# Kernel tuning notes

Hardware: AMD Instinct MI355X
Metric: run time of the kernel (lower is better)

Reference implementation:

```python
import jax, jax.numpy as jnp
import numpy as np

B, S, D, E = 4, 2048, 512, 32

def setup_inputs() -> dict:
    key = jax.random.key(0)
    k1, k2, k3 = jax.random.split(key, 3)
    x = jax.random.normal(k1, (B, S, D), dtype=jnp.float32)
    # glorot-ish scaling for weights
    gate_w = jax.random.normal(k2, (D, E), dtype=jnp.float32) * (1.0 / np.sqrt(D))
    gate_b = jnp.zeros((E,), dtype=jnp.float32)
    expert_w = jax.random.normal(k3, (E, D, D), dtype=jnp.float32) * (1.0 / np.sqrt(D))
    return {"x": x, "gate_w": gate_w, "gate_b": gate_b, "expert_w": expert_w}

def reference(x, gate_w, gate_b, expert_w):
    # gate_scores: [B,S,E] (context=None -> route on x itself)
    gate = jax.nn.softmax(jnp.einsum('bsd,de->bse', x, gate_w) + gate_b, axis=-1)
    # Dense soft-MoE: sum_e gate[b,s,e] * (x[b,s,:] @ expert_w[e])
    # Single einsum avoids materializing the [B,S,E,D] intermediate.
    out = jnp.einsum('bse,bsd,edf->bsf', gate, x, expert_w)
    return out
```

## Files before the change

kernel.cpp:

```cpp
#include <hip/hip_runtime.h>

#define TOK 8192
#define DIM 512
#define NE  32
#define KTOT (NE * DIM)

#define BM 128
#define BN 128
#define BK 64

typedef float f32x4  __attribute__((ext_vector_type(4)));
typedef float f32x16 __attribute__((ext_vector_type(16)));
typedef short s16x8  __attribute__((ext_vector_type(8)));

typedef const void __attribute__((address_space(1)))* gp1_t;
typedef void __attribute__((address_space(3)))* lp3_t;

__device__ __forceinline__ void gl_lds16(const void* g, void* l) {
    __builtin_amdgcn_global_load_lds((gp1_t)g, (lp3_t)l, 16, 0, 0);
}

__device__ __forceinline__ void stage4(const ushort* g, size_t gstride, char* l) {
    gl_lds16(g,               l);
    gl_lds16(g + gstride,     l + 4096);
    gl_lds16(g + 2 * gstride, l + 8192);
    gl_lds16(g + 3 * gstride, l + 12288);
}

__device__ __forceinline__ ushort f2bf(float f) {
    unsigned u = __builtin_bit_cast(unsigned, f);
    unsigned r = (u + 0x7fffu + ((u >> 16) & 1u)) >> 16;
    return (ushort)r;
}

__global__ __launch_bounds__(256) void k_prep(const float* __restrict__ w,
                                              ushort* __restrict__ wt,
                                              const float* __restrict__ x,
                                              const float* __restrict__ gw,
                                              const float* __restrict__ gb,
                                              float* __restrict__ G,
                                              ushort* __restrict__ xb) {
    __shared__ __align__(16) char smem[64 * 65 * 4];
    const int bx = blockIdx.x;
    const int tid = threadIdx.x;
    if (bx < 2048) {
        float (*tile)[65] = (float(*)[65])smem;
        const int e = bx >> 6;
        const int f0 = ((bx >> 3) & 7) * 64;
        const int d0 = (bx & 7) * 64;
        const int tx = tid & 63, ty = tid >> 6;
        const float* we = w + (size_t)e * DIM * DIM;
#pragma unroll
        for (int i = ty; i < 64; i += 4)
            tile[i][tx] = we[(size_t)(d0 + i) * DIM + f0 + tx];
        __syncthreads();
#pragma unroll
        for (int i = ty; i < 64; i += 4)
            wt[(size_t)(f0 + i) * KTOT + e * DIM + d0 + tx] = f2bf(tile[tx][i]);
    } else {
        float* xs = (float*)smem;
        const int t0 = (bx - 2048) * 8;
        const float* xBase = x + (size_t)t0 * DIM;
#pragma unroll
        for (int k = 0; k < 4; ++k) {
            int i4 = (k * 256 + tid) * 4;
            float4 v = *(const float4*)(xBase + i4);
            xs[i4 + 0] = v.x; xs[i4 + 1] = v.y; xs[i4 + 2] = v.z; xs[i4 + 3] = v.w;
            ushort4 o;
            o.x = f2bf(v.x); o.y = f2bf(v.y); o.z = f2bf(v.z); o.w = f2bf(v.w);
            *(ushort4*)(xb + (size_t)t0 * DIM + i4) = o;
        }
        __syncthreads();
        const int tok = tid >> 5;
        const int e = tid & 31;
        float l = gb[e];
        const float* xr = xs + tok * DIM;
#pragma unroll 8
        for (int d = 0; d < DIM; ++d)
            l += xr[d] * gw[d * NE + e];
        float mx = l;
#pragma unroll
        for (int m = 16; m >= 1; m >>= 1) mx = fmaxf(mx, __shfl_xor(mx, m));
        float ex = expf(l - mx);
        float s = ex;
#pragma unroll
        for (int m = 16; m >= 1; m >>= 1) s += __shfl_xor(s, m);
        G[(size_t)(t0 + tok) * NE + e] = ex / s;
    }
}

__global__ __launch_bounds__(256, 2) void k_moe_gemm(const ushort* __restrict__ xb,
                                                     const ushort* __restrict__ wt,
                                                     const float* __restrict__ G,
                                                     float* __restrict__ out0,
                                                     float* __restrict__ out1) {
    __shared__ __align__(16) ushort As[2][BM * BK];
    __shared__ __align__(16) ushort Bs[2][BN * BK];
    __shared__ float Gs[16][BM];

    const int tid = threadIdx.x;
    const int m0 = blockIdx.y * BM;
    const int n0 = blockIdx.x * BN;
    const int e0 = blockIdx.z * 16;
    float* __restrict__ dst = blockIdx.z ? out1 : out0;

    for (int i = tid; i < 16 * BM; i += 256) {
        int e = i >> 7, r = i & 127;
        Gs[e][r] = G[(size_t)(m0 + r) * NE + e0 + e];
    }

    const int lane = tid & 63;
    const int wave = tid >> 6;
    const int wm = (wave & 1) * 64;
    const int wn = (wave >> 1) * 64;
    const int l31 = lane & 31;
    const int hi = lane >> 5;
    const int key = l31 & 7;

    int chunkOff[4], rowOffA[2], rowOffB[2];
#pragma unroll
    for (int s = 0; s < 4; ++s) chunkOff[s] = ((2 * s + hi) ^ key) * 16;
#pragma unroll
    for (int i = 0; i < 2; ++i) {
        rowOffA[i] = (wm + i * 32 + l31) * 128;
        rowOffB[i] = (wn + i * 32 + l31) * 128;
    }

    const int srow = tid >> 3;
    const int scol = ((tid & 7) ^ (srow & 7)) * 8;
    const ushort* aBase = xb + (size_t)(m0 + srow) * DIM + scol;
    const ushort* bBase = wt + (size_t)(n0 + srow) * KTOT + (size_t)e0 * DIM + scol;
    const int ldsOff = tid * 16;

    f32x16 zv16;
#pragma unroll
    for (int j = 0; j < 16; ++j) zv16[j] = 0.f;
    f32x16 acc[2][2];
#pragma unroll
    for (int i = 0; i < 2; ++i)
#pragma unroll
        for (int j = 0; j < 2; ++j) acc[i][j] = zv16;

    stage4(aBase, (size_t)32 * DIM,  (char*)As[0] + ldsOff);
    stage4(bBase, (size_t)32 * KTOT, (char*)Bs[0] + ldsOff);
    __syncthreads();

#pragma unroll 1
    for (int kt = 0; kt < 8; ++kt) {
        const char* Ab = (const char*)As[kt & 1];
        s16x8 areg[2][4];
#pragma unroll
        for (int mi = 0; mi < 2; ++mi)
#pragma unroll
            for (int s = 0; s < 4; ++s)
                areg[mi][s] = *(const s16x8*)(Ab + rowOffA[mi] + chunkOff[s]);

#pragma unroll 1
        for (int ee = 0; ee < 16; ++ee) {
            const int gn = kt * 16 + ee + 1;
            if (gn < 128) {
                const ushort* bN = bBase + (size_t)(gn & 15) * DIM + (gn >> 4) * BK;
                stage4(bN, (size_t)32 * KTOT, (char*)Bs[gn & 1] + ldsOff);
                if (ee == 15)
                    stage4(aBase + (gn >> 4) * BK, (size_t)32 * DIM,
                           (char*)As[(gn >> 4) & 1] + ldsOff);
            }

            const char* Bb = (const char*)Bs[ee & 1];
            s16x8 breg[2][4];
#pragma unroll
            for (int nj = 0; nj < 2; ++nj)
#pragma unroll
                for (int s = 0; s < 4; ++s)
                    breg[nj][s] = *(const s16x8*)(Bb + rowOffB[nj] + chunkOff[s]);

#pragma unroll
            for (int mi = 0; mi < 2; ++mi) {
                f32x16 p0 = __builtin_amdgcn_mfma_f32_32x32x16_bf16(areg[mi][0], breg[0][0], zv16, 0, 0, 0);
                f32x16 p1 = __builtin_amdgcn_mfma_f32_32x32x16_bf16(areg[mi][0], breg[1][0], zv16, 0, 0, 0);
#pragma unroll
                for (int s = 1; s < 4; ++s) {
                    p0 = __builtin_amdgcn_mfma_f32_32x32x16_bf16(areg[mi][s], breg[0][s], p0, 0, 0, 0);
                    p1 = __builtin_amdgcn_mfma_f32_32x32x16_bf16(areg[mi][s], breg[1][s], p1, 0, 0, 0);
                }
#pragma unroll
                for (int g = 0; g < 4; ++g) {
                    const f32x4 gt = *(const f32x4*)&Gs[ee][wm + mi * 32 + 8 * g + 4 * hi];
#pragma unroll
                    for (int j = 0; j < 4; ++j) {
                        acc[mi][0][4 * g + j] += gt[j] * p0[4 * g + j];
                        acc[mi][1][4 * g + j] += gt[j] * p1[4 * g + j];
                    }
                }
            }
            __syncthreads();
        }
    }

#pragma unroll
    for (int mi = 0; mi < 2; ++mi)
#pragma unroll
        for (int nj = 0; nj < 2; ++nj) {
            const int col = n0 + wn + nj * 32 + l31;
#pragma unroll
            for (int g = 0; g < 4; ++g) {
                float* p = dst + (size_t)(m0 + wm + mi * 32 + 8 * g + 4 * hi) * DIM + col;
                p[0 * DIM] = acc[mi][nj][4 * g + 0];
                p[1 * DIM] = acc[mi][nj][4 * g + 1];
                p[2 * DIM] = acc[mi][nj][4 * g + 2];
                p[3 * DIM] = acc[mi][nj][4 * g + 3];
            }
        }
}

__global__ __launch_bounds__(256) void k_reduce(float* __restrict__ out,
                                                const float* __restrict__ P) {
    int i = (blockIdx.x * 256 + threadIdx.x) * 4;
    float4 a = *(const float4*)(out + i);
    float4 b = *(const float4*)(P + i);
    a.x += b.x; a.y += b.y; a.z += b.z; a.w += b.w;
    *(float4*)(out + i) = a;
}

extern "C" void kernel_launch(void* const* d_in, const int* in_sizes, int n_in,
                              void* d_out, int out_size, void* d_ws, size_t ws_size,
                              hipStream_t stream) {
    const float* x  = (const float*)d_in[0];
    const float* gw = (const float*)d_in[1];
    const float* gb = (const float*)d_in[2];
    const float* w  = (const float*)d_in[3];
    float* out = (float*)d_out;

    char* ws = (char*)d_ws;
    ushort* xb = (ushort*)ws;
    ushort* wt = (ushort*)(ws + (8u << 20));
    float*  G  = (float*)(ws + (24u << 20));
    float*  P  = (float*)(ws + (25u << 20));

    k_prep<<<dim3(2048 + TOK / 8), dim3(256), 0, stream>>>(w, wt, x, gw, gb, G, xb);
    k_moe_gemm<<<dim3(DIM / BN, TOK / BM, 2), dim3(256), 0, stream>>>(xb, wt, G, out, P);
    k_reduce<<<dim3(TOK * DIM / 1024), dim3(256), 0, stream>>>(out, P);
}
```

Baseline: 259.9 us.

## Triple-buffer B tiles with prefetch distance two and counted vmcnt waits

The GEMM's B-tile staging moves from double to triple buffering, and loads are issued two iterations ahead. The full __syncthreads is replaced with s_waitcnt vmcnt(N) plus a barrier, so in-flight global-to-LDS loads can keep running across iterations. The A tile becomes single-buffered and is reloaded once per kt, after its registers have been read. This targets memory-latency stalls, at the cost of extra LDS per block, which may reduce occupancy. It also depends on precise vmcnt accounting being correct.

Measured after the change: 284.3 us. +9.4%, slower.

```diff
diff --git a/kernel.cpp b/kernel.cpp
--- a/kernel.cpp
+++ b/kernel.cpp
@@ -25,6 +25,12 @@
     gl_lds16(g + gstride,     l + 4096);
     gl_lds16(g + 2 * gstride, l + 8192);
     gl_lds16(g + 3 * gstride, l + 12288);
+}
+
+template<int N>
+__device__ __forceinline__ void wait_bar() {
+    asm volatile("s_waitcnt vmcnt(%0) lgkmcnt(0)" :: "n"(N) : "memory");
+    __builtin_amdgcn_s_barrier();
 }
 
 __device__ __forceinline__ ushort f2bf(float f) {
@@ -94,8 +100,8 @@
                                                      const float* __restrict__ G,
                                                      float* __restrict__ out0,
                                                      float* __restrict__ out1) {
-    __shared__ __align__(16) ushort As[2][BM * BK];
-    __shared__ __align__(16) ushort Bs[2][BN * BK];
+    __shared__ __align__(16) ushort As[BM * BK];
+    __shared__ __align__(16) ushort Bs[3][BN * BK];
     __shared__ float Gs[16][BM];
 
     const int tid = threadIdx.x;
@@ -141,38 +147,50 @@
 #pragma unroll
         for (int j = 0; j < 2; ++j) acc[i][j] = zv16;
 
-    stage4(aBase, (size_t)32 * DIM,  (char*)As[0] + ldsOff);
+    stage4(aBase, (size_t)32 * DIM, (char*)As + ldsOff);
     stage4(bBase, (size_t)32 * KTOT, (char*)Bs[0] + ldsOff);
-    __syncthreads();
+    stage4(bBase + (size_t)1 * DIM, (size_t)32 * KTOT, (char*)Bs[1] + ldsOff);
+    asm volatile("s_waitcnt vmcnt(0) lgkmcnt(0)" ::: "memory");
+    __builtin_amdgcn_s_barrier();
+
+    char* Br0 = (char*)Bs[0];
+    char* Br1 = (char*)Bs[1];
+    char* Br2 = (char*)Bs[2];
+
+    s16x8 areg[2][4];
 
 #pragma unroll 1
     for (int kt = 0; kt < 8; ++kt) {
-        const char* Ab = (const char*)As[kt & 1];
-        s16x8 areg[2][4];
-#pragma unroll
-        for (int mi = 0; mi < 2; ++mi)
-#pragma unroll
-            for (int s = 0; s < 4; ++s)
-                areg[mi][s] = *(const s16x8*)(Ab + rowOffA[mi] + chunkOff[s]);
-
 #pragma unroll 1
         for (int ee = 0; ee < 16; ++ee) {
-            const int gn = kt * 16 + ee + 1;
+            const int g = kt * 16 + ee;
+
+            if (kt == 7 && ee == 15)                  wait_bar<0>();
+            else if (kt < 7 && (ee == 2 || ee == 3))  wait_bar<8>();
+            else                                      wait_bar<4>();
+
+            const int gn = g + 2;
             if (gn < 128) {
                 const ushort* bN = bBase + (size_t)(gn & 15) * DIM + (gn >> 4) * BK;
-                stage4(bN, (size_t)32 * KTOT, (char*)Bs[gn & 1] + ldsOff);
-                if (ee == 15)
-                    stage4(aBase + (gn >> 4) * BK, (size_t)32 * DIM,
-                           (char*)As[(gn >> 4) & 1] + ldsOff);
-            }
-
-            const char* Bb = (const char*)Bs[ee & 1];
+                stage4(bN, (size_t)32 * KTOT, Br2 + ldsOff);
+            }
+            if (ee == 1 && kt < 7)
+                stage4(aBase + (kt + 1) * BK, (size_t)32 * DIM, (char*)As + ldsOff);
+
+            if (ee == 0) {
+#pragma unroll
+                for (int mi = 0; mi < 2; ++mi)
+#pragma unroll
+                    for (int s = 0; s < 4; ++s)
+                        areg[mi][s] = *(const s16x8*)((const char*)As + rowOffA[mi] + chunkOff[s]);
+            }
+
             s16x8 breg[2][4];
 #pragma unroll
             for (int nj = 0; nj < 2; ++nj)
 #pragma unroll
                 for (int s = 0; s < 4; ++s)
-                    breg[nj][s] = *(const s16x8*)(Bb + rowOffB[nj] + chunkOff[s]);
+                    breg[nj][s] = *(const s16x8*)(Br0 + rowOffB[nj] + chunkOff[s]);
 
 #pragma unroll
             for (int mi = 0; mi < 2; ++mi) {
@@ -184,16 +202,17 @@
                     p1 = __builtin_amdgcn_mfma_f32_32x32x16_bf16(areg[mi][s], breg[1][s], p1, 0, 0, 0);
                 }
 #pragma unroll
-                for (int g = 0; g < 4; ++g) {
-                    const f32x4 gt = *(const f32x4*)&Gs[ee][wm + mi * 32 + 8 * g + 4 * hi];
+                for (int gq = 0; gq < 4; ++gq) {
+                    const f32x4 gt = *(const f32x4*)&Gs[ee][wm + mi * 32 + 8 * gq + 4 * hi];
 #pragma unroll
                     for (int j = 0; j < 4; ++j) {
-                        acc[mi][0][4 * g + j] += gt[j] * p0[4 * g + j];
-                        acc[mi][1][4 * g + j] += gt[j] * p1[4 * g + j];
+                        acc[mi][0][4 * gq + j] += gt[j] * p0[4 * gq + j];
+                        acc[mi][1][4 * gq + j] += gt[j] * p1[4 * gq + j];
                     }
                 }
             }
-            __syncthreads();
+
+            char* t = Br0; Br0 = Br1; Br1 = Br2; Br2 = t;
         }
     }
 
@@ -203,12 +222,12 @@
         for (int nj = 0; nj < 2; ++nj) {
             const int col = n0 + wn + nj * 32 + l31;
 #pragma unroll
-            for (int g = 0; g < 4; ++g) {
-                float* p = dst + (size_t)(m0 + wm + mi * 32 + 8 * g + 4 * hi) * DIM + col;
-                p[0 * DIM] = acc[mi][nj][4 * g + 0];
-                p[1 * DIM] = acc[mi][nj][4 * g + 1];
-                p[2 * DIM] = acc[mi][nj][4 * g + 2];
-                p[3 * DIM] = acc[mi][nj][4 * g + 3];
+            for (int gq = 0; gq < 4; ++gq) {
+                float* p = dst + (size_t)(m0 + wm + mi * 32 + 8 * gq + 4 * hi) * DIM + col;
+                p[0 * DIM] = acc[mi][nj][4 * gq + 0];
+                p[1 * DIM] = acc[mi][nj][4 * gq + 1];
+                p[2 * DIM] = acc[mi][nj][4 * gq + 2];
+                p[3 * DIM] = acc[mi][nj][4 * gq + 3];
             }
         }
 }
```

## Double GEMM M-tile to 256 rows with 512-thread blocks

Applied to the files above, without the earlier changes.

Raises the MoE GEMM row tile from 128 to 256 tokens and launches 8 waves per block, arranged 4 along M and 2 along N. The staging helpers are rewritten for the new row strides. Each staged B tile of expert weights is now reused across twice as many tokens, which halves the B-operand global and LDS traffic per output. The cost is more LDS per block and fewer blocks in the grid (256 instead of 512), which may lower occupancy and load balance across the CUs.

New measurement: 262.1 us. About the same (+0.9%).

```diff
diff --git a/kernel.cpp b/kernel.cpp
--- a/kernel.cpp
+++ b/kernel.cpp
@@ -5,7 +5,7 @@
 #define NE  32
 #define KTOT (NE * DIM)
 
-#define BM 128
+#define BM 256
 #define BN 128
 #define BK 64
 
@@ -20,11 +20,15 @@
     __builtin_amdgcn_global_load_lds((gp1_t)g, (lp3_t)l, 16, 0, 0);
 }
 
-__device__ __forceinline__ void stage4(const ushort* g, size_t gstride, char* l) {
-    gl_lds16(g,               l);
-    gl_lds16(g + gstride,     l + 4096);
-    gl_lds16(g + 2 * gstride, l + 8192);
-    gl_lds16(g + 3 * gstride, l + 12288);
+__device__ __forceinline__ void stageA(const ushort* g, char* l) {
+    gl_lds16(g,                      l);
+    gl_lds16(g + (size_t) 64 * DIM,  l + 8192);
+    gl_lds16(g + (size_t)128 * DIM,  l + 16384);
+    gl_lds16(g + (size_t)192 * DIM,  l + 24576);
+}
+__device__ __forceinline__ void stageB(const ushort* g, char* l) {
+    gl_lds16(g,                      l);
+    gl_lds16(g + (size_t)64 * KTOT,  l + 8192);
 }
 
 __device__ __forceinline__ ushort f2bf(float f) {
@@ -89,7 +93,7 @@
     }
 }
 
-__global__ __launch_bounds__(256, 2) void k_moe_gemm(const ushort* __restrict__ xb,
+__global__ __launch_bounds__(512, 2) void k_moe_gemm(const ushort* __restrict__ xb,
                                                      const ushort* __restrict__ wt,
                                                      const float* __restrict__ G,
                                                      float* __restrict__ out0,
@@ -104,15 +108,15 @@
     const int e0 = blockIdx.z * 16;
     float* __restrict__ dst = blockIdx.z ? out1 : out0;
 
-    for (int i = tid; i < 16 * BM; i += 256) {
-        int e = i >> 7, r = i & 127;
+    for (int i = tid; i < 16 * BM; i += 512) {
+        int e = i >> 8, r = i & 255;
         Gs[e][r] = G[(size_t)(m0 + r) * NE + e0 + e];
     }
 
     const int lane = tid & 63;
     const int wave = tid >> 6;
-    const int wm = (wave & 1) * 64;
-    const int wn = (wave >> 1) * 64;
+    const int wm = (wave & 3) * 64;
+    const int wn = (wave >> 2) * 64;
     const int l31 = lane & 31;
     const int hi = lane >> 5;
     const int key = l31 & 7;
@@ -141,8 +145,8 @@
 #pragma unroll
         for (int j = 0; j < 2; ++j) acc[i][j] = zv16;
 
-    stage4(aBase, (size_t)32 * DIM,  (char*)As[0] + ldsOff);
-    stage4(bBase, (size_t)32 * KTOT, (char*)Bs[0] + ldsOff);
+    stageA(aBase, (char*)As[0] + ldsOff);
+    stageB(bBase, (char*)Bs[0] + ldsOff);
     __syncthreads();
 
 #pragma unroll 1
@@ -160,10 +164,9 @@
             const int gn = kt * 16 + ee + 1;
             if (gn < 128) {
                 const ushort* bN = bBase + (size_t)(gn & 15) * DIM + (gn >> 4) * BK;
-                stage4(bN, (size_t)32 * KTOT, (char*)Bs[gn & 1] + ldsOff);
+                stageB(bN, (char*)Bs[gn & 1] + ldsOff);
                 if (ee == 15)
-                    stage4(aBase + (gn >> 4) * BK, (size_t)32 * DIM,
-                           (char*)As[(gn >> 4) & 1] + ldsOff);
+                    stageA(aBase + (kt + 1) * BK, (char*)As[(kt + 1) & 1] + ldsOff);
             }
 
             const char* Bb = (const char*)Bs[ee & 1];
@@ -184,12 +187,12 @@
                     p1 = __builtin_amdgcn_mfma_f32_32x32x16_bf16(areg[mi][s], breg[1][s], p1, 0, 0, 0);
                 }
 #pragma unroll
-                for (int g = 0; g < 4; ++g) {
-                    const f32x4 gt = *(const f32x4*)&Gs[ee][wm + mi * 32 + 8 * g + 4 * hi];
+                for (int gq = 0; gq < 4; ++gq) {
+                    const f32x4 gt = *(const f32x4*)&Gs[ee][wm + mi * 32 + 8 * gq + 4 * hi];
 #pragma unroll
                     for (int j = 0; j < 4; ++j) {
-                        acc[mi][0][4 * g + j] += gt[j] * p0[4 * g + j];
-                        acc[mi][1][4 * g + j] += gt[j] * p1[4 * g + j];
+                        acc[mi][0][4 * gq + j] += gt[j] * p0[4 * gq + j];
+                        acc[mi][1][4 * gq + j] += gt[j] * p1[4 * gq + j];
                     }
                 }
             }
@@ -203,12 +206,12 @@
         for (int nj = 0; nj < 2; ++nj) {
             const int col = n0 + wn + nj * 32 + l31;
 #pragma unroll
-            for (int g = 0; g < 4; ++g) {
-                float* p = dst + (size_t)(m0 + wm + mi * 32 + 8 * g + 4 * hi) * DIM + col;
-                p[0 * DIM] = acc[mi][nj][4 * g + 0];
-                p[1 * DIM] = acc[mi][nj][4 * g + 1];
-                p[2 * DIM] = acc[mi][nj][4 * g + 2];
-                p[3 * DIM] = acc[mi][nj][4 * g + 3];
+            for (int gq = 0; gq < 4; ++gq) {
+                float* p = dst + (size_t)(m0 + wm + mi * 32 + 8 * gq + 4 * hi) * DIM + col;
+                p[0 * DIM] = acc[mi][nj][4 * gq + 0];
+                p[1 * DIM] = acc[mi][nj][4 * gq + 1];
+                p[2 * DIM] = acc[mi][nj][4 * gq + 2];
+                p[3 * DIM] = acc[mi][nj][4 * gq + 3];
             }
         }
 }
@@ -238,6 +241,6 @@
     float*  P  = (float*)(ws + (25u << 20));
 
     k_prep<<<dim3(2048 + TOK / 8), dim3(256), 0, stream>>>(w, wt, x, gw, gb, G, xb);
-    k_moe_gemm<<<dim3(DIM / BN, TOK / BM, 2), dim3(256), 0, stream>>>(xb, wt, G, out, P);
+    k_moe_gemm<<<dim3(DIM / BN, TOK / BM, 2), dim3(512), 0, stream>>>(xb, wt, G, out, P);
     k_reduce<<<dim3(TOK * DIM / 1024), dim3(256), 0, stream>>>(out, P);
 }
```
